# Kernel optimization log

Measured on AMD Instinct MI355X. Metric: run time of the kernel, lower is better.

The kernel has to match this reference:

```python
import jax, jax.numpy as jnp
import numpy as np

N_QUBITS = 10
N_LAYERS = 3
DIM = 2 ** N_QUBITS
B = 2048
T1, T2, GATE_TIME = 0.05, 0.07, 1e-07
P_GATE_1Q, P_GATE_2Q, P_READOUT = 0.001, 0.01, 0.02
P_AMP = 1.0 - np.exp(-GATE_TIME / T1)
P_PHASE = 1.0 - np.exp(-GATE_TIME / T2)

_I = np.eye(2, dtype=np.complex64)
_X = np.array([[0, 1], [1, 0]], np.complex64)
_Y = np.array([[0, -1j], [1j, 0]], np.complex64)
_Z = np.array([[1, 0], [0, -1]], np.complex64)

def _depol(p):
    return [np.sqrt(1 - p) * _I, np.sqrt(p / 3) * _X, np.sqrt(p / 3) * _Y, np.sqrt(p / 3) * _Z]

def _ampdamp(g):
    return [np.array([[1, 0], [0, np.sqrt(1 - g)]], np.complex64), np.array([[0, np.sqrt(g)], [0, 0]], np.complex64)]

def _phasedamp(g):
    return [np.array([[1, 0], [0, np.sqrt(1 - g)]], np.complex64), np.array([[0, 0], [0, np.sqrt(g)]], np.complex64)]

def _bitflip(p):
    return [np.sqrt(1 - p) * _I, np.sqrt(p) * _X]

DEPOL1 = [jnp.asarray(k) for k in _depol(P_GATE_1Q)]
DEPOL2 = [jnp.asarray(k) for k in _depol(P_GATE_2Q)]
AMP = [jnp.asarray(k) for k in _ampdamp(P_AMP)]
PHASE = [jnp.asarray(k) for k in _phasedamp(P_PHASE)]
BITFLIP = [jnp.asarray(k) for k in _bitflip(P_READOUT)]
CNOT = jnp.asarray(np.array([[1, 0, 0, 0], [0, 1, 0, 0], [0, 0, 0, 1], [0, 0, 1, 0]], np.complex64).reshape(2, 2, 2, 2))

def pauli_strings(n):
    out = []
    for q in range(n):
        for ch in 'XZ':
            out.append('I' * q + ch + 'I' * (n - q - 1))
    return out

def pauli_tensor(strings):
    mats = {'I': np.eye(2), 'X': np.array([[0., 1.], [1., 0.]]), 'Z': np.array([[1., 0.], [0., -1.]])}
    Ps = []
    for s in strings:
        P = np.array([[1.0]])
        for ch in s:
            P = np.kron(P, mats[ch])
        Ps.append(P)
    return np.stack(Ps).astype(np.float32)

def _apply1(rho, K, q, n):
    # rho' = K rho K^dagger on wire q; rho has shape (2,)*2n (ket axes 0..n-1, bra axes n..2n-1)
    rho = jnp.moveaxis(jnp.tensordot(K, rho, axes=[[1], [q]]), 0, q)
    rho = jnp.moveaxis(jnp.tensordot(jnp.conj(K), rho, axes=[[1], [n + q]]), 0, n + q)
    return rho

def _apply2(rho, U, q1, q2, n):
    rho = jnp.moveaxis(jnp.tensordot(U, rho, axes=[[2, 3], [q1, q2]]), [0, 1], [q1, q2])
    rho = jnp.moveaxis(jnp.tensordot(jnp.conj(U), rho, axes=[[2, 3], [n + q1, n + q2]]), [0, 1], [n + q1, n + q2])
    return rho

def _chan1(rho, Ks, q, n):
    out = _apply1(rho, Ks[0], q, n)
    for K in Ks[1:]:
        out = out + _apply1(rho, K, q, n)
    return out

def _rot(phi, theta, omega):
    # qml.Rot = RZ(omega) @ RY(theta) @ RZ(phi)
    c = jnp.cos(theta / 2).astype(jnp.complex64)
    s = jnp.sin(theta / 2).astype(jnp.complex64)
    ep = jnp.exp(-0.5j * (phi + omega))
    em = jnp.exp(0.5j * (phi - omega))
    return jnp.stack([jnp.stack([ep * c, -em * s]), jnp.stack([jnp.conj(em) * s, jnp.conj(ep) * c])])

def _simulate(weights):
    nl, nq, _ = weights.shape
    rho = jnp.zeros((2,) * (2 * nq), jnp.complex64).at[(0,) * (2 * nq)].set(1.0)
    for l in range(nl):
        for q in range(nq):
            rho = _apply1(rho, _rot(weights[l, q, 0], weights[l, q, 1], weights[l, q, 2]), q, nq)
            rho = _chan1(rho, DEPOL1, q, nq)
            rho = _chan1(rho, AMP, q, nq)
            rho = _chan1(rho, PHASE, q, nq)
        for q in range(nq):
            t = (q + 1) % nq
            rho = _apply2(rho, CNOT, q, t, nq)
            for wq in (q, t):
                rho = _chan1(rho, DEPOL2, wq, nq)
            for wq in (q, t):
                rho = _chan1(rho, AMP, wq, nq)
            for wq in (q, t):
                rho = _chan1(rho, PHASE, wq, nq)
    for q in range(nq):
        rho = _chan1(rho, BITFLIP, q, nq)
    return rho.reshape(2 ** nq, 2 ** nq)

def setup_inputs() -> dict:
    key = jax.random.key(0)
    k1, k2, k3 = jax.random.split(key, 3)
    x = jax.random.normal(k1, (B, DIM), jnp.float32)
    circuit_weights = jax.random.uniform(k2, (N_LAYERS, N_QUBITS, 3), jnp.float32)
    w = jax.random.normal(k3, (2 * N_QUBITS,), jnp.float32) * 0.01
    b = jnp.zeros((DIM,), jnp.float32)
    P_tensor = jnp.asarray(pauli_tensor(pauli_strings(N_QUBITS)))  # [K, dim, dim]
    return {"x": x, "b": b, "w": w, "circuit_weights": circuit_weights, "P_tensor": P_tensor}

def reference(x, b, w, circuit_weights, P_tensor):
    x_t = x + b  # [B, dim]
    feats = jnp.einsum('bm,kmn,bn->bk', x_t, P_tensor, x_t)  # [B, K]
    rho = _simulate(circuit_weights)  # [dim, dim] complex
    exps = jnp.real(jnp.einsum('kmn,nm->k', P_tensor.astype(jnp.complex64), rho))  # tr(P_k rho)
    logits = jnp.sum(feats * (w * exps), axis=1)
    return jax.nn.sigmoid(logits)
```

## Files before the change

### kernel.cpp

```cpp
#include <hip/hip_runtime.h>
#include <hip/hip_bf16.h>
#include <math.h>

struct cf { float x, y; };
__device__ __forceinline__ cf cfmul(cf a, cf b){ return {a.x*b.x - a.y*b.y, a.x*b.y + a.y*b.x}; }
__device__ __forceinline__ cf cfconj(cf a){ return {a.x, -a.y}; }
__device__ __forceinline__ cf cfadd(cf a, cf b){ return {a.x+b.x, a.y+b.y}; }

__device__ __forceinline__ void pmat(int k, cf* P){
    if (k==0){ P[0]={1.f,0.f}; P[1]={0.f,0.f}; P[2]={0.f,0.f}; P[3]={1.f,0.f}; }
    else if (k==1){ P[0]={0.f,0.f}; P[1]={1.f,0.f}; P[2]={1.f,0.f}; P[3]={0.f,0.f}; }
    else if (k==2){ P[0]={0.f,0.f}; P[1]={0.f,-1.f}; P[2]={0.f,1.f}; P[3]={0.f,0.f}; }
    else { P[0]={1.f,0.f}; P[1]={0.f,0.f}; P[2]={0.f,0.f}; P[3]={-1.f,0.f}; }
}
__device__ void mul2(cf* C, const cf* A, const cf* B){
    C[0]=cfadd(cfmul(A[0],B[0]),cfmul(A[1],B[2]));
    C[1]=cfadd(cfmul(A[0],B[1]),cfmul(A[1],B[3]));
    C[2]=cfadd(cfmul(A[2],B[0]),cfmul(A[3],B[2]));
    C[3]=cfadd(cfmul(A[2],B[1]),cfmul(A[3],B[3]));
}
__device__ void ptm_acc(float* T, const cf* K){
    cf Kd[4] = {cfconj(K[0]), cfconj(K[2]), cfconj(K[1]), cfconj(K[3])};
    for (int s=0;s<4;s++){
        cf Ps[4]; pmat(s,Ps);
        cf t1[4], t2[4];
        mul2(t1, K, Ps);
        mul2(t2, t1, Kd);
        for (int t=0;t<4;t++){
            cf Pt[4]; pmat(t,Pt);
            float re = Pt[0].x*t2[0].x - Pt[0].y*t2[0].y
                     + Pt[1].x*t2[2].x - Pt[1].y*t2[2].y
                     + Pt[2].x*t2[1].x - Pt[2].y*t2[1].y
                     + Pt[3].x*t2[3].x - Pt[3].y*t2[3].y;
            T[t*4+s] += 0.5f*re;
        }
    }
}
__device__ void rmm4(float* C, const float* A, const float* B){
    for (int i=0;i<4;i++) for (int j=0;j<4;j++){
        float s=0.f;
        for (int k=0;k<4;k++) s += A[i*4+k]*B[k*4+j];
        C[i*4+j]=s;
    }
}

__device__ void prep_sm(float* sm, const float* __restrict__ wts, int tid){
    if (tid < 31){
        const float GA = -expm1f(-2.0000000000000002e-06f);
        const float GP = -expm1f(-1.4285714285714286e-06f);
        float sa = sqrtf(1.f-GA), spp = sqrtf(1.f-GP);
        float p = (tid==30) ? 0.01f : 0.001f;
        float f = 1.f - (4.f/3.f)*p;
        float Tn[16] = {0};
        Tn[0]      = 1.f;
        Tn[1*4+1]  = spp*sa*f;
        Tn[2*4+2]  = spp*sa*f;
        Tn[3*4+3]  = (1.f-GA)*f;
        Tn[3*4+0]  = GA;
        if (tid == 30){
            for (int i=0;i<16;i++) sm[480+i] = Tn[i];
        } else {
            float phi = wts[tid*3+0], th = wts[tid*3+1], om = wts[tid*3+2];
            float ct = cosf(0.5f*th), st = sinf(0.5f*th);
            cf ep = {cosf(0.5f*(phi+om)), -sinf(0.5f*(phi+om))};
            cf em = {cosf(0.5f*(phi-om)),  sinf(0.5f*(phi-om))};
            cf U[4];
            U[0] = { ep.x*ct,  ep.y*ct};
            U[1] = {-em.x*st, -em.y*st};
            U[2] = { em.x*st, -em.y*st};
            U[3] = { ep.x*ct, -ep.y*ct};
            float Tr[16] = {0};
            ptm_acc(Tr, U);
            float S[16]; rmm4(S, Tn, Tr);
            for (int i=0;i<16;i++) sm[tid*16+i] = S[i];
        }
    }
}

__device__ __forceinline__ unsigned swz(unsigned t){ return t ^ ((t>>7)&0x1Cu); }

#define ALONG_A(Mp) { _Pragma("unroll") for (int db_=0; db_<4; db_++){ \
    float a0=v[db_], a1=v[4+db_], a2=v[8+db_], a3=v[12+db_]; \
    _Pragma("unroll") for (int dp_=0; dp_<4; dp_++){ \
        v[dp_*4+db_] = (Mp)[dp_*4+0]*a0 + (Mp)[dp_*4+1]*a1 + (Mp)[dp_*4+2]*a2 + (Mp)[dp_*4+3]*a3; } } }

#define ALONG_B(Mp) { _Pragma("unroll") for (int da_=0; da_<4; da_++){ \
    float a0=v[da_*4+0], a1=v[da_*4+1], a2=v[da_*4+2], a3=v[da_*4+3]; \
    _Pragma("unroll") for (int dp_=0; dp_<4; dp_++){ \
        v[da_*4+dp_] = (Mp)[dp_*4+0]*a0 + (Mp)[dp_*4+1]*a1 + (Mp)[dp_*4+2]*a2 + (Mp)[dp_*4+3]*a3; } } }

template<int LAYER, int ISB, int DOINIT, int MODE>
__global__ void __launch_bounds__(256)
fused6(float* __restrict__ rho, const float* __restrict__ wts, float* __restrict__ cvec)
{
    __shared__ __align__(16) float tile[4096];
    __shared__ float sm[31*16];
    int tid = threadIdx.x;
    unsigned blk = blockIdx.x;
    if (MODE == 2){
        const unsigned LUT[9] = {0,1,3,4,12,16,48,64,192};
        blk = LUT[blockIdx.x];
    }

    prep_sm(sm, wts, tid);

    unsigned bo = blk << (ISB ? 4 : 12);
    if (DOINIT){
#pragma unroll
        for (int r=0; r<16; r++){
            unsigned u = tid + 256u*r;
            unsigned g = u | bo;
            unsigned e = g & 0x55555u, o = (g>>1) & 0x55555u;
            tile[swz(u)] = (e==o) ? 1.f : 0.f;
        }
    } else {
#pragma unroll
        for (int r=0; r<4; r++){
            unsigned u = 4u*(tid + 256u*r);
            unsigned g = ISB ? ((u & 15u) | ((u>>4)<<12) | bo) : (u | bo);
            *reinterpret_cast<float4*>(&tile[swz(u)]) = *reinterpret_cast<const float4*>(rho + g);
        }
    }
    __syncthreads();

    constexpr int A_PA[5] = {0,10,8,6,4}, A_PB[5] = {10,8,6,4,2};
    constexpr int B_PA[5] = {2,10,8,6,4}, B_PB[5] = {10,8,6,4,0};

#pragma unroll
    for (int i=0; i<5; i++){
        const int pa = ISB ? B_PA[i] : A_PA[i];
        const int pb = ISB ? B_PB[i] : A_PB[i];
        const int mA = (!ISB && i==0) ? LAYER*160 : -1;
        const int mB = !ISB ? (LAYER*10 + i + 1)*16
                            : ((i < 4) ? (LAYER*10 + 6 + i)*16 : -1);
        const int lo = pa < pb ? pa : pb, hi = pa < pb ? pb : pa;
        unsigned g8 = (unsigned)tid;
        unsigned xx = ((g8 >> lo) << (lo+2)) | (g8 & ((1u<<lo)-1u));
        xx = ((xx >> hi) << (hi+2)) | (xx & ((1u<<hi)-1u));
        unsigned adr[16];
        float v[16];
#pragma unroll
        for (int d=0; d<16; d++){
            unsigned t = xx | ((unsigned)(d>>2) << pa) | ((unsigned)(d&3) << pb);
            adr[d] = swz(t);
            v[d] = tile[adr[d]];
        }
        if (mA >= 0){ const float* M = sm + mA; ALONG_A(M); }
        if (mB >= 0){ const float* M = sm + mB; ALONG_B(M); }
        {
            float t0;
            t0=v[4];  v[4]=v[5];   v[5]=t0;
            t0=v[8];  v[8]=v[9];   v[9]=t0;
            t0=v[2];  v[2]=v[14];  v[14]=t0;
            t0=v[3];  v[3]=v[15];  v[15]=t0;
            t0=v[6];  v[6]=v[11];  v[11]=t0;
            t0=v[7];  v[7]=-v[10]; v[10]=-t0;
        }
        { const float* M = sm + 480; ALONG_B(M); ALONG_A(M); }
#pragma unroll
        for (int d=0; d<16; d++) tile[adr[d]] = v[d];
        __syncthreads();
    }

    if (MODE != 2){
#pragma unroll
        for (int r=0; r<4; r++){
            unsigned u = 4u*(tid + 256u*r);
            unsigned g = ISB ? ((u & 15u) | ((u>>4)<<12) | bo) : (u | bo);
            *reinterpret_cast<float4*>(rho + g) = *reinterpret_cast<const float4*>(&tile[swz(u)]);
        }
        return;
    }

    if (blk == 0){
        if (tid < 12){
            const int TQ[6] = {0,5,9,8,7,6};
            int i = tid >> 1, isZ = tid & 1;
            unsigned u = (isZ ? 3u : 1u) << (2*i);
            cvec[2*TQ[i] + isZ] = tile[swz(u)];
        }
    } else if (tid == 0){
        const int BQ[4] = {4,3,2,1};
#pragma unroll
        for (int j=0; j<4; j++){
            if (blk == (1u<<(2*j))) cvec[2*BQ[j]]   = tile[0];
            if (blk == (3u<<(2*j))) cvec[2*BQ[j]+1] = tile[0];
        }
    }
}

__global__ void __launch_bounds__(256)
logits_kernel(const float* __restrict__ x, const float* __restrict__ bvec,
              const float* __restrict__ cvec, const float* __restrict__ w,
              float* __restrict__ out)
{
    __shared__ float xs[1024];
    __shared__ float cX[10], cZ[10];
    __shared__ float red[4];
    int b = blockIdx.x, tid = threadIdx.x;
    if (tid < 10){
        cX[tid] = w[2*tid] * cvec[2*tid];
        cZ[tid] = 0.96f * w[2*tid+1] * cvec[2*tid+1];
    }
    {
        float4 xv = reinterpret_cast<const float4*>(x + (size_t)b*1024)[tid];
        float4 bv = reinterpret_cast<const float4*>(bvec)[tid];
        xs[tid*4+0] = xv.x + bv.x;
        xs[tid*4+1] = xv.y + bv.y;
        xs[tid*4+2] = xv.z + bv.z;
        xs[tid*4+3] = xv.w + bv.w;
    }
    __syncthreads();
    float acc = 0.f;
#pragma unroll
    for (int r=0; r<4; r++){
        int m = tid + r*256;
        float xm = xs[m];
        float sd = 0.f;
#pragma unroll
        for (int qq=0; qq<10; qq++){
            float cz = cZ[qq];
            sd += (m & (1<<(9-qq))) ? -cz : cz;
            acc += cX[qq] * xm * xs[m ^ (1<<(9-qq))];
        }
        acc += sd * xm * xm;
    }
    for (int o=32; o>0; o>>=1) acc += __shfl_down(acc, o);
    if ((tid & 63) == 0) red[tid>>6] = acc;
    __syncthreads();
    if (tid == 0){
        float l = red[0]+red[1]+red[2]+red[3];
        out[b] = 1.f / (1.f + expf(-l));
    }
}

extern "C" void kernel_launch(void* const* d_in, const int* in_sizes, int n_in,
                              void* d_out, int out_size, void* d_ws, size_t ws_size,
                              hipStream_t stream) {
    const float* x    = (const float*)d_in[0];
    const float* bvec = (const float*)d_in[1];
    const float* w    = (const float*)d_in[2];
    const float* cw   = (const float*)d_in[3];
    float* out = (float*)d_out;

    char* ws = (char*)d_ws;
    float* rho  = (float*)ws;
    float* cvec = (float*)(ws + (size_t)(1u<<20)*sizeof(float));
    (void)ws_size; (void)in_sizes; (void)n_in; (void)out_size;

    fused6<0,0,1,0><<<256, 256, 0, stream>>>(rho, cw, cvec);
    fused6<0,1,0,0><<<256, 256, 0, stream>>>(rho, cw, cvec);
    fused6<1,0,0,0><<<256, 256, 0, stream>>>(rho, cw, cvec);
    fused6<1,1,0,0><<<256, 256, 0, stream>>>(rho, cw, cvec);
    fused6<2,0,0,0><<<256, 256, 0, stream>>>(rho, cw, cvec);
    fused6<2,1,0,2><<<9,   256, 0, stream>>>(rho, cw, cvec);
    logits_kernel<<<2048, 256, 0, stream>>>(x, bvec, cvec, w, out);
}
```

Baseline: 66.41 us.

## Fuse final density-matrix stage into logits kernel with atomic ticket sync

Merges the last 9-block simulation stage and the logits kernel into one launch. The first 9 blocks to grab an atomic ticket finish the circuit and write the expectation values, while every block computes per-qubit X/Z feature sums independently and then spins on a counter before combining them. The previous layer now writes back only the 36 rho entries the tail needs instead of the full tile. This removes one kernel launch and lets feature computation overlap the tail simulation, at the cost of a spin-wait that depends on the ticket blocks being scheduled and a larger per-block reduction.

```diff
diff --git a/kernel.cpp b/kernel.cpp
--- a/kernel.cpp
+++ b/kernel.cpp
@@ -89,43 +89,10 @@
     _Pragma("unroll") for (int dp_=0; dp_<4; dp_++){ \
         v[da_*4+dp_] = (Mp)[dp_*4+0]*a0 + (Mp)[dp_*4+1]*a1 + (Mp)[dp_*4+2]*a2 + (Mp)[dp_*4+3]*a3; } } }
 
-template<int LAYER, int ISB, int DOINIT, int MODE>
-__global__ void __launch_bounds__(256)
-fused6(float* __restrict__ rho, const float* __restrict__ wts, float* __restrict__ cvec)
-{
-    __shared__ __align__(16) float tile[4096];
-    __shared__ float sm[31*16];
-    int tid = threadIdx.x;
-    unsigned blk = blockIdx.x;
-    if (MODE == 2){
-        const unsigned LUT[9] = {0,1,3,4,12,16,48,64,192};
-        blk = LUT[blockIdx.x];
-    }
-
-    prep_sm(sm, wts, tid);
-
-    unsigned bo = blk << (ISB ? 4 : 12);
-    if (DOINIT){
-#pragma unroll
-        for (int r=0; r<16; r++){
-            unsigned u = tid + 256u*r;
-            unsigned g = u | bo;
-            unsigned e = g & 0x55555u, o = (g>>1) & 0x55555u;
-            tile[swz(u)] = (e==o) ? 1.f : 0.f;
-        }
-    } else {
-#pragma unroll
-        for (int r=0; r<4; r++){
-            unsigned u = 4u*(tid + 256u*r);
-            unsigned g = ISB ? ((u & 15u) | ((u>>4)<<12) | bo) : (u | bo);
-            *reinterpret_cast<float4*>(&tile[swz(u)]) = *reinterpret_cast<const float4*>(rho + g);
-        }
-    }
-    __syncthreads();
-
+template<int LAYER, int ISB>
+__device__ __forceinline__ void run_ops(float* tile, const float* sm, int tid){
     constexpr int A_PA[5] = {0,10,8,6,4}, A_PB[5] = {10,8,6,4,2};
     constexpr int B_PA[5] = {2,10,8,6,4}, B_PB[5] = {10,8,6,4,0};
-
 #pragma unroll
     for (int i=0; i<5; i++){
         const int pa = ISB ? B_PA[i] : A_PA[i];
@@ -161,49 +128,116 @@
         for (int d=0; d<16; d++) tile[adr[d]] = v[d];
         __syncthreads();
     }
-
-    if (MODE != 2){
+}
+
+template<int LAYER, int ISB, int DOINIT, int MODE>
+__global__ void __launch_bounds__(256)
+fused6(float* __restrict__ rho, const float* __restrict__ wts, unsigned* __restrict__ sync)
+{
+    __shared__ __align__(16) float tile[4096];
+    __shared__ float sm[31*16];
+    int tid = threadIdx.x;
+    unsigned blk = blockIdx.x;
+
+    prep_sm(sm, wts, tid);
+
+    unsigned bo = blk << (ISB ? 4 : 12);
+    if (DOINIT){
+#pragma unroll
+        for (int r=0; r<16; r++){
+            unsigned u = tid + 256u*r;
+            unsigned g = u | bo;
+            unsigned e = g & 0x55555u, o = (g>>1) & 0x55555u;
+            tile[swz(u)] = (e==o) ? 1.f : 0.f;
+        }
+    } else {
 #pragma unroll
         for (int r=0; r<4; r++){
             unsigned u = 4u*(tid + 256u*r);
             unsigned g = ISB ? ((u & 15u) | ((u>>4)<<12) | bo) : (u | bo);
-            *reinterpret_cast<float4*>(rho + g) = *reinterpret_cast<const float4*>(&tile[swz(u)]);
+            *reinterpret_cast<float4*>(&tile[swz(u)]) = *reinterpret_cast<const float4*>(rho + g);
+        }
+    }
+    __syncthreads();
+
+    run_ops<LAYER, ISB>(tile, sm, tid);
+
+    if (MODE == 3){
+        if (blk == 0 && tid == 0){ sync[0] = 0u; sync[1] = 0u; }
+        if (tid < 36){
+            const unsigned LUT9[9] = {0,1,3,4,12,16,48,64,192};
+            unsigned u = (LUT9[tid>>2] << 4) | ((tid & 3u) << 2);
+            *reinterpret_cast<float4*>(rho + (u | bo)) =
+                *reinterpret_cast<const float4*>(&tile[swz(u)]);
         }
         return;
     }
 
-    if (blk == 0){
-        if (tid < 12){
-            const int TQ[6] = {0,5,9,8,7,6};
-            int i = tid >> 1, isZ = tid & 1;
-            unsigned u = (isZ ? 3u : 1u) << (2*i);
-            cvec[2*TQ[i] + isZ] = tile[swz(u)];
-        }
-    } else if (tid == 0){
-        const int BQ[4] = {4,3,2,1};
-#pragma unroll
-        for (int j=0; j<4; j++){
-            if (blk == (1u<<(2*j))) cvec[2*BQ[j]]   = tile[0];
-            if (blk == (3u<<(2*j))) cvec[2*BQ[j]+1] = tile[0];
-        }
+#pragma unroll
+    for (int r=0; r<4; r++){
+        unsigned u = 4u*(tid + 256u*r);
+        unsigned g = ISB ? ((u & 15u) | ((u>>4)<<12) | bo) : (u | bo);
+        *reinterpret_cast<float4*>(rho + g) = *reinterpret_cast<const float4*>(&tile[swz(u)]);
     }
 }
 
 __global__ void __launch_bounds__(256)
-logits_kernel(const float* __restrict__ x, const float* __restrict__ bvec,
-              const float* __restrict__ cvec, const float* __restrict__ w,
-              float* __restrict__ out)
+mega_tail(float* __restrict__ rho, const float* __restrict__ wts,
+          float* __restrict__ cvec, unsigned* __restrict__ sync,
+          const float* __restrict__ x, const float* __restrict__ bvec,
+          const float* __restrict__ w, float* __restrict__ out)
 {
-    __shared__ float xs[1024];
-    __shared__ float cX[10], cZ[10];
-    __shared__ float red[4];
-    int b = blockIdx.x, tid = threadIdx.x;
-    if (tid < 10){
-        cX[tid] = w[2*tid] * cvec[2*tid];
-        cZ[tid] = 0.96f * w[2*tid+1] * cvec[2*tid+1];
-    }
+    __shared__ __align__(16) float tile[4096];
+    __shared__ float sm[31*16];
+    __shared__ float redl[80];
+    __shared__ unsigned sticket;
+    int tid = threadIdx.x;
+    unsigned bid = blockIdx.x;
+
+    if (tid == 0)
+        sticket = __hip_atomic_fetch_add(&sync[1], 1u, __ATOMIC_RELAXED, __HIP_MEMORY_SCOPE_AGENT);
+    __syncthreads();
+    unsigned t = sticket;
+
+    if (t < 9u){
+        const unsigned LUT9[9] = {0,1,3,4,12,16,48,64,192};
+        unsigned blk = LUT9[t];
+        prep_sm(sm, wts, tid);
+        unsigned bo = blk << 4;
+#pragma unroll
+        for (int r=0; r<4; r++){
+            unsigned u = 4u*(tid + 256u*r);
+            unsigned g = (u & 15u) | ((u>>4)<<12) | bo;
+            *reinterpret_cast<float4*>(&tile[swz(u)]) = *reinterpret_cast<const float4*>(rho + g);
+        }
+        __syncthreads();
+        run_ops<2, 1>(tile, sm, tid);
+        if (blk == 0){
+            if (tid < 12){
+                const int TQ[6] = {0,5,9,8,7,6};
+                int i = tid >> 1, isZ = tid & 1;
+                unsigned u = (isZ ? 3u : 1u) << (2*i);
+                cvec[2*TQ[i] + isZ] = tile[swz(u)];
+            }
+        } else if (tid == 0){
+            const int BQ[4] = {4,3,2,1};
+#pragma unroll
+            for (int j=0; j<4; j++){
+                if (blk == (1u<<(2*j))) cvec[2*BQ[j]]   = tile[0];
+                if (blk == (3u<<(2*j))) cvec[2*BQ[j]+1] = tile[0];
+            }
+        }
+        __syncthreads();
+        if (tid == 0){
+            __threadfence();
+            __hip_atomic_fetch_add(&sync[0], 1u, __ATOMIC_RELEASE, __HIP_MEMORY_SCOPE_AGENT);
+        }
+        __syncthreads();
+    }
+
+    float* xs = tile;
     {
-        float4 xv = reinterpret_cast<const float4*>(x + (size_t)b*1024)[tid];
+        float4 xv = reinterpret_cast<const float4*>(x + (size_t)bid*1024)[tid];
         float4 bv = reinterpret_cast<const float4*>(bvec)[tid];
         xs[tid*4+0] = xv.x + bv.x;
         xs[tid*4+1] = xv.y + bv.y;
@@ -211,26 +245,43 @@
         xs[tid*4+3] = xv.w + bv.w;
     }
     __syncthreads();
-    float acc = 0.f;
+    float aX[10] = {0,0,0,0,0,0,0,0,0,0};
+    float aZ[10] = {0,0,0,0,0,0,0,0,0,0};
 #pragma unroll
     for (int r=0; r<4; r++){
         int m = tid + r*256;
         float xm = xs[m];
-        float sd = 0.f;
-#pragma unroll
-        for (int qq=0; qq<10; qq++){
-            float cz = cZ[qq];
-            sd += (m & (1<<(9-qq))) ? -cz : cz;
-            acc += cX[qq] * xm * xs[m ^ (1<<(9-qq))];
-        }
-        acc += sd * xm * xm;
-    }
-    for (int o=32; o>0; o>>=1) acc += __shfl_down(acc, o);
-    if ((tid & 63) == 0) red[tid>>6] = acc;
+        float x2 = xm*xm;
+#pragma unroll
+        for (int q=0; q<10; q++){
+            int bit = 1 << (9-q);
+            aX[q] += xm * xs[m ^ bit];
+            aZ[q] += (m & bit) ? -x2 : x2;
+        }
+    }
+    int lane = tid & 63, wv = tid >> 6;
+#pragma unroll
+    for (int k=0; k<20; k++){
+        float v = (k < 10) ? aX[k] : aZ[k-10];
+        v += __shfl_down(v, 32); v += __shfl_down(v, 16); v += __shfl_down(v, 8);
+        v += __shfl_down(v, 4);  v += __shfl_down(v, 2);  v += __shfl_down(v, 1);
+        if (lane == 0) redl[wv*20 + k] = v;
+    }
     __syncthreads();
+
     if (tid == 0){
-        float l = red[0]+red[1]+red[2]+red[3];
-        out[b] = 1.f / (1.f + expf(-l));
+        while (__hip_atomic_load(&sync[0], __ATOMIC_ACQUIRE, __HIP_MEMORY_SCOPE_AGENT) < 9u)
+            __builtin_amdgcn_s_sleep(8);
+        __threadfence();
+        float logit = 0.f;
+#pragma unroll
+        for (int q=0; q<10; q++){
+            float FX = redl[q]    + redl[20+q] + redl[40+q] + redl[60+q];
+            float FZ = redl[10+q] + redl[30+q] + redl[50+q] + redl[70+q];
+            logit += w[2*q]   * cvec[2*q]   * FX
+                   + 0.96f * w[2*q+1] * cvec[2*q+1] * FZ;
+        }
+        out[bid] = 1.f / (1.f + expf(-logit));
     }
 }
 
@@ -244,15 +295,15 @@
     float* out = (float*)d_out;
 
     char* ws = (char*)d_ws;
-    float* rho  = (float*)ws;
-    float* cvec = (float*)(ws + (size_t)(1u<<20)*sizeof(float));
+    float*    rho  = (float*)ws;
+    float*    cvec = (float*)(ws + (size_t)(1u<<20)*sizeof(float));
+    unsigned* sync = (unsigned*)(ws + (size_t)(1u<<20)*sizeof(float) + 128);
     (void)ws_size; (void)in_sizes; (void)n_in; (void)out_size;
 
-    fused6<0,0,1,0><<<256, 256, 0, stream>>>(rho, cw, cvec);
-    fused6<0,1,0,0><<<256, 256, 0, stream>>>(rho, cw, cvec);
-    fused6<1,0,0,0><<<256, 256, 0, stream>>>(rho, cw, cvec);
-    fused6<1,1,0,0><<<256, 256, 0, stream>>>(rho, cw, cvec);
-    fused6<2,0,0,0><<<256, 256, 0, stream>>>(rho, cw, cvec);
-    fused6<2,1,0,2><<<9,   256, 0, stream>>>(rho, cw, cvec);
-    logits_kernel<<<2048, 256, 0, stream>>>(x, bvec, cvec, w, out);
-}
+    fused6<0,0,1,0><<<256, 256, 0, stream>>>(rho, cw, sync);
+    fused6<0,1,0,0><<<256, 256, 0, stream>>>(rho, cw, sync);
+    fused6<1,0,0,0><<<256, 256, 0, stream>>>(rho, cw, sync);
+    fused6<1,1,0,0><<<256, 256, 0, stream>>>(rho, cw, sync);
+    fused6<2,0,0,3><<<256, 256, 0, stream>>>(rho, cw, sync);
+    mega_tail<<<2048, 256, 0, stream>>>(rho, cw, cvec, sync, x, bvec, w, out);
+}
```

Measured after the change: 161.3 us. 143% more time.
